# Optimization experiments

Measured on AMD Instinct MI355X. Metric: run time of the kernel, lower is better.

## Reference

```python
import jax, jax.numpy as jnp
import numpy as np

SKIP = 91
PREEMPH = 0.85
N = 33554432  # 2**25 samples


def setup_inputs() -> dict:
    key = jax.random.key(0)
    sig = jax.random.normal(key, (N,), dtype=jnp.float32) * 0.1
    return {"sig": sig}


def _preemph_scan(y, coef):
    # First-order IIR: out[0] = y[0]; out[i] = y[i] + coef * out[i-1]
    # Expressed as an associative scan over pairs (a, b) representing x -> a*x + b.
    a = jnp.full_like(y, coef)

    def combine(e1, e2):
        a1, b1 = e1
        a2, b2 = e2
        return a1 * a2, b2 + a2 * b1

    _, out = jax.lax.associative_scan(combine, (a, y))
    return out


def reference(sig):
    y = _preemph_scan(sig, jnp.float32(PREEMPH))
    # drop first `skip` samples, zero-pad the tail (same length)
    y = jnp.concatenate([y[SKIP:], jnp.zeros((SKIP,), dtype=y.dtype)])
    out = jnp.clip(32768.0 * y, -32768.0, 32767.0).astype(jnp.int16)
    return out
```

## Files before the change

### kernel.cpp

```cpp
#include <hip/hip_runtime.h>


#define BLOCK   256
#define SKIP    91
#define COEF    0.85f
#define CHUNK_N 256
#define CHUNKS  8
#define SEG     (CHUNKS * CHUNK_N)
#define WPB     (BLOCK / 64)
#define TILE    (WPB * SEG)

typedef int v4i __attribute__((ext_vector_type(4)));

__device__ __forceinline__ int cvt16(float v) {
    float s = v * 32768.f;
    s = fminf(fmaxf(s, -32768.f), 32767.f);
    return (int)s;
}

__device__ __forceinline__ float4 ld_guard(const float* __restrict__ sig,
                                           long yb, long n) {
    float4 x;
    x.x = (yb + 0 >= 0 && yb + 0 < n) ? sig[yb + 0] : 0.f;
    x.y = (yb + 1 >= 0 && yb + 1 < n) ? sig[yb + 1] : 0.f;
    x.z = (yb + 2 >= 0 && yb + 2 < n) ? sig[yb + 2] : 0.f;
    x.w = (yb + 3 >= 0 && yb + 3 < n) ? sig[yb + 3] : 0.f;
    return x;
}

template <bool FAST>
__device__ __forceinline__ void run_seg(const float* __restrict__ sig,
                                        int* __restrict__ out,
                                        long segBase, long ln, int lane) {
    const float K1  = COEF * COEF * COEF * COEF;
    const float K2  = K1 * K1;
    const float K4  = K2 * K2;
    const float K8  = K4 * K4;
    const float K16 = K8 * K8;
    const float KS[5] = {K1, K2, K4, K8, K16};
    const float C1 = COEF, C2 = COEF * COEF, C3 = C2 * COEF;
    const float wq = exp2f((float)lane * (4.0f * -0.23446525109f));

    float4 x[9];
    if constexpr (FAST) {
        const float* base = sig + segBase + 4 * (long)lane;
#pragma unroll
        for (int c = 0; c < 8; ++c)
            x[c] = *reinterpret_cast<const float4*>(base + (SKIP + 1) + c * CHUNK_N);
        x[8] = *reinterpret_cast<const float4*>(base - 164);
    } else {
#pragma unroll
        for (int c = 0; c < 8; ++c)
            x[c] = ld_guard(sig, segBase + (SKIP + 1) + (long)c * CHUNK_N
                                 + 4 * (long)lane, ln);
        x[8] = ld_guard(sig, segBase - 164 + 4 * (long)lane, ln);
    }

    float t[9], s0[8], s1[8], s2[8];
#pragma unroll
    for (int c = 0; c < 9; ++c) {
        float a0 = x[c].x;
        float a1 = fmaf(a0, COEF, x[c].y);
        float a2 = fmaf(a1, COEF, x[c].z);
        float a3 = fmaf(a2, COEF, x[c].w);
        if (c < 8) { s0[c] = a0; s1[c] = a1; s2[c] = a2; }
        t[c] = a3;
    }

#pragma unroll
    for (int d = 0; d < 5; ++d) {
        const int sh = 1 << d;
        float u[9];
#pragma unroll
        for (int c = 0; c < 9; ++c) u[c] = __shfl_up(t[c], sh, 64);
#pragma unroll
        for (int c = 0; c < 9; ++c)
            t[c] = (lane >= sh) ? fmaf(u[c], KS[d], t[c]) : t[c];
    }

    float tsh[8], Tp[8];
#pragma unroll
    for (int c = 0; c < 8; ++c) tsh[c] = __shfl_up(t[c], 1, 64);
#pragma unroll
    for (int c = 0; c < 8; ++c) Tp[c] = __shfl(t[c == 0 ? 8 : c - 1], 63, 64);

    const long oLim = ln - SKIP;
#pragma unroll
    for (int c = 0; c < 8; ++c) {
        float u = (lane == 0) ? 0.f : tsh[c];
        float p = fmaf(Tp[c], wq, u);
        v4i iv;
        iv.x = cvt16(p);
        iv.y = cvt16(fmaf(p, C1, s0[c]));
        iv.z = cvt16(fmaf(p, C2, s1[c]));
        iv.w = cvt16(fmaf(p, C3, s2[c]));
        const long ob = segBase + (long)c * CHUNK_N + 4 * (long)lane;
        if constexpr (FAST) {
            *reinterpret_cast<v4i*>(out + ob) = iv;
        } else {
            if (ob + 0 >= oLim) iv.x = 0;
            if (ob + 1 >= oLim) iv.y = 0;
            if (ob + 2 >= oLim) iv.z = 0;
            if (ob + 3 >= oLim) iv.w = 0;
            if (ob + 0 < ln) out[ob + 0] = iv.x;
            if (ob + 1 < ln) out[ob + 1] = iv.y;
            if (ob + 2 < ln) out[ob + 2] = iv.z;
            if (ob + 3 < ln) out[ob + 3] = iv.w;
        }
    }
}

__global__ __launch_bounds__(BLOCK, 6) void preemph_kernel(
        const float* __restrict__ sig, int* __restrict__ out, int n) {
    const long ln   = n;
    const int  lane = threadIdx.x & 63;
    const long segBase = (long)blockIdx.x * TILE + (long)(threadIdx.x >> 6) * SEG;
    if (segBase >= ln) return;

    const bool fast = (segBase >= 164) && (segBase + SEG + SKIP + 1 <= ln);
    if (fast) run_seg<true >(sig, out, segBase, ln, lane);
    else      run_seg<false>(sig, out, segBase, ln, lane);
}

extern "C" void kernel_launch(void* const* d_in, const int* in_sizes, int n_in,
                              void* d_out, int out_size, void* d_ws, size_t ws_size,
                              hipStream_t stream) {
    const float* sig = (const float*)d_in[0];
    int* out = (int*)d_out;
    int n = in_sizes[0];
    int grid = (int)(((long)n + TILE - 1) / TILE);
    preemph_kernel<<<grid, BLOCK, 0, stream>>>(sig, out, n);
}
```

Measured before the change: 231.6 us.

## Stage fast-path input through LDS with direct global-to-LDS loads

On the fast path each wave now fetches its nine 256-float windows with global_load_lds straight into a per-wave shared-memory buffer, waits on vmcnt, then reads float4s back from LDS for the scan. The partial prefix values s0/s1/s2 are recomputed at output time instead of being kept in registers, and the guarded path is split into a separate non-templated function. Launch bounds drop from 6 to 4 waves per EU, trading occupancy for register headroom. The aim is to cut VGPR pressure and make the global loads more efficient. The cost is an extra LDS round trip and a full vmcnt wait that serialises load and compute within each wave.

```diff
diff --git a/kernel.cpp b/kernel.cpp
--- a/kernel.cpp
+++ b/kernel.cpp
@@ -9,13 +9,40 @@
 #define SEG     (CHUNKS * CHUNK_N)
 #define WPB     (BLOCK / 64)
 #define TILE    (WPB * SEG)
+#define NW      9
+#define WFLOATS (NW * CHUNK_N)
 
 typedef int v4i __attribute__((ext_vector_type(4)));
+typedef __attribute__((address_space(3))) void       as3_void;
+typedef const __attribute__((address_space(1))) void as1_void;
 
 __device__ __forceinline__ int cvt16(float v) {
     float s = v * 32768.f;
     s = fminf(fmaxf(s, -32768.f), 32767.f);
     return (int)s;
+}
+
+__device__ __forceinline__ float chain4(const float4& v) {
+    float a1 = fmaf(v.x, COEF, v.y);
+    float a2 = fmaf(a1, COEF, v.z);
+    return fmaf(a2, COEF, v.w);
+}
+
+template <int N>
+__device__ __forceinline__ void wscan_multi(float (&t)[N], int lane) {
+    const float K1  = COEF * COEF * COEF * COEF;
+    const float K2  = K1 * K1, K4 = K2 * K2, K8 = K4 * K4, K16 = K8 * K8;
+    const float KS[5] = {K1, K2, K4, K8, K16};
+#pragma unroll
+    for (int d = 0; d < 5; ++d) {
+        const int sh = 1 << d;
+        float u[N];
+#pragma unroll
+        for (int c = 0; c < N; ++c) u[c] = __shfl_up(t[c], sh, 64);
+#pragma unroll
+        for (int c = 0; c < N; ++c)
+            t[c] = (lane >= sh) ? fmaf(u[c], KS[d], t[c]) : t[c];
+    }
 }
 
 __device__ __forceinline__ float4 ld_guard(const float* __restrict__ sig,
@@ -28,98 +55,100 @@
     return x;
 }
 
-template <bool FAST>
-__device__ __forceinline__ void run_seg(const float* __restrict__ sig,
-                                        int* __restrict__ out,
-                                        long segBase, long ln, int lane) {
-    const float K1  = COEF * COEF * COEF * COEF;
-    const float K2  = K1 * K1;
-    const float K4  = K2 * K2;
-    const float K8  = K4 * K4;
-    const float K16 = K8 * K8;
-    const float KS[5] = {K1, K2, K4, K8, K16};
+__device__ void run_guard(const float* __restrict__ sig, int* __restrict__ out,
+                          long segBase, long ln, int lane, float wq) {
     const float C1 = COEF, C2 = COEF * COEF, C3 = C2 * COEF;
-    const float wq = exp2f((float)lane * (4.0f * -0.23446525109f));
-
     float4 x[9];
-    if constexpr (FAST) {
-        const float* base = sig + segBase + 4 * (long)lane;
 #pragma unroll
-        for (int c = 0; c < 8; ++c)
-            x[c] = *reinterpret_cast<const float4*>(base + (SKIP + 1) + c * CHUNK_N);
-        x[8] = *reinterpret_cast<const float4*>(base - 164);
-    } else {
+    for (int c = 0; c < 8; ++c)
+        x[c] = ld_guard(sig, segBase + (SKIP + 1) + (long)c * CHUNK_N
+                             + 4 * (long)lane, ln);
+    x[8] = ld_guard(sig, segBase - 164 + 4 * (long)lane, ln);
+    float t[9];
 #pragma unroll
-        for (int c = 0; c < 8; ++c)
-            x[c] = ld_guard(sig, segBase + (SKIP + 1) + (long)c * CHUNK_N
-                                 + 4 * (long)lane, ln);
-        x[8] = ld_guard(sig, segBase - 164 + 4 * (long)lane, ln);
-    }
-
-    float t[9], s0[8], s1[8], s2[8];
-#pragma unroll
-    for (int c = 0; c < 9; ++c) {
-        float a0 = x[c].x;
-        float a1 = fmaf(a0, COEF, x[c].y);
-        float a2 = fmaf(a1, COEF, x[c].z);
-        float a3 = fmaf(a2, COEF, x[c].w);
-        if (c < 8) { s0[c] = a0; s1[c] = a1; s2[c] = a2; }
-        t[c] = a3;
-    }
-
-#pragma unroll
-    for (int d = 0; d < 5; ++d) {
-        const int sh = 1 << d;
-        float u[9];
-#pragma unroll
-        for (int c = 0; c < 9; ++c) u[c] = __shfl_up(t[c], sh, 64);
-#pragma unroll
-        for (int c = 0; c < 9; ++c)
-            t[c] = (lane >= sh) ? fmaf(u[c], KS[d], t[c]) : t[c];
-    }
-
+    for (int c = 0; c < 9; ++c) t[c] = chain4(x[c]);
+    wscan_multi<9>(t, lane);
     float tsh[8], Tp[8];
 #pragma unroll
     for (int c = 0; c < 8; ++c) tsh[c] = __shfl_up(t[c], 1, 64);
 #pragma unroll
     for (int c = 0; c < 8; ++c) Tp[c] = __shfl(t[c == 0 ? 8 : c - 1], 63, 64);
-
     const long oLim = ln - SKIP;
 #pragma unroll
     for (int c = 0; c < 8; ++c) {
-        float u = (lane == 0) ? 0.f : tsh[c];
-        float p = fmaf(Tp[c], wq, u);
+        float u  = (lane == 0) ? 0.f : tsh[c];
+        float p  = fmaf(Tp[c], wq, u);
+        float s1 = fmaf(x[c].x, COEF, x[c].y);
+        float s2 = fmaf(s1, COEF, x[c].z);
         v4i iv;
         iv.x = cvt16(p);
-        iv.y = cvt16(fmaf(p, C1, s0[c]));
-        iv.z = cvt16(fmaf(p, C2, s1[c]));
-        iv.w = cvt16(fmaf(p, C3, s2[c]));
+        iv.y = cvt16(fmaf(p, C1, x[c].x));
+        iv.z = cvt16(fmaf(p, C2, s1));
+        iv.w = cvt16(fmaf(p, C3, s2));
         const long ob = segBase + (long)c * CHUNK_N + 4 * (long)lane;
-        if constexpr (FAST) {
-            *reinterpret_cast<v4i*>(out + ob) = iv;
-        } else {
-            if (ob + 0 >= oLim) iv.x = 0;
-            if (ob + 1 >= oLim) iv.y = 0;
-            if (ob + 2 >= oLim) iv.z = 0;
-            if (ob + 3 >= oLim) iv.w = 0;
-            if (ob + 0 < ln) out[ob + 0] = iv.x;
-            if (ob + 1 < ln) out[ob + 1] = iv.y;
-            if (ob + 2 < ln) out[ob + 2] = iv.z;
-            if (ob + 3 < ln) out[ob + 3] = iv.w;
-        }
+        if (ob + 0 >= oLim) iv.x = 0;
+        if (ob + 1 >= oLim) iv.y = 0;
+        if (ob + 2 >= oLim) iv.z = 0;
+        if (ob + 3 >= oLim) iv.w = 0;
+        if (ob + 0 < ln) out[ob + 0] = iv.x;
+        if (ob + 1 < ln) out[ob + 1] = iv.y;
+        if (ob + 2 < ln) out[ob + 2] = iv.z;
+        if (ob + 3 < ln) out[ob + 3] = iv.w;
     }
 }
 
-__global__ __launch_bounds__(BLOCK, 6) void preemph_kernel(
+__global__ __launch_bounds__(BLOCK, 4) void preemph_kernel(
         const float* __restrict__ sig, int* __restrict__ out, int n) {
+    __shared__ float lds[WPB][WFLOATS];
     const long ln   = n;
     const int  lane = threadIdx.x & 63;
-    const long segBase = (long)blockIdx.x * TILE + (long)(threadIdx.x >> 6) * SEG;
+    const int  wid  = threadIdx.x >> 6;
+    const long segBase = (long)blockIdx.x * TILE + (long)wid * SEG;
     if (segBase >= ln) return;
 
+    const float wq = exp2f((float)lane * (4.0f * -0.23446525109f));
+
     const bool fast = (segBase >= 164) && (segBase + SEG + SKIP + 1 <= ln);
-    if (fast) run_seg<true >(sig, out, segBase, ln, lane);
-    else      run_seg<false>(sig, out, segBase, ln, lane);
+    if (!fast) { run_guard(sig, out, segBase, ln, lane, wq); return; }
+
+    const float* gsrc = sig + (segBase - 164) + 4 * (long)lane;
+    float* lb = &lds[wid][0];
+#pragma unroll
+    for (int w = 0; w < NW; ++w)
+        __builtin_amdgcn_global_load_lds((as1_void*)(gsrc + w * CHUNK_N),
+                                         (as3_void*)(lb + w * CHUNK_N),
+                                         16, 0, 0);
+    asm volatile("s_waitcnt vmcnt(0)" ::: "memory");
+    __builtin_amdgcn_sched_barrier(0);
+
+    float4 xw[NW];
+    const float* lr = lb + 4 * lane;
+#pragma unroll
+    for (int w = 0; w < NW; ++w)
+        xw[w] = *reinterpret_cast<const float4*>(lr + w * CHUNK_N);
+
+    float t[NW];
+#pragma unroll
+    for (int w = 0; w < NW; ++w) t[w] = chain4(xw[w]);
+    wscan_multi<NW>(t, lane);
+
+    const float C1 = COEF, C2 = COEF * COEF, C3 = C2 * COEF;
+#pragma unroll
+    for (int c = 0; c < CHUNKS; ++c) {
+        float tsh = __shfl_up(t[c + 1], 1, 64);
+        float Tp  = __shfl(t[c], 63, 64);
+        float u   = (lane == 0) ? 0.f : tsh;
+        float p   = fmaf(Tp, wq, u);
+        const float4 x = xw[c + 1];
+        float s1 = fmaf(x.x, COEF, x.y);
+        float s2 = fmaf(s1, COEF, x.z);
+        v4i iv;
+        iv.x = cvt16(p);
+        iv.y = cvt16(fmaf(p, C1, x.x));
+        iv.z = cvt16(fmaf(p, C2, s1));
+        iv.w = cvt16(fmaf(p, C3, s2));
+        *reinterpret_cast<v4i*>(out + segBase + c * CHUNK_N + 4 * (long)lane) = iv;
+    }
 }
 
 extern "C" void kernel_launch(void* const* d_in, const int* in_sizes, int n_in,
```

Result: no change. 231.8 us (+0.1%).
